# Kernel tuning notes

Measured on AMD Instinct MI355X. Metric: run time of the kernel, lower is better.

## Reference

```python
import jax, jax.numpy as jnp
import numpy as np

N = 50000      # nodes
E = 800000     # edges (before self-loops)
IN_DIM = 256
HID = 128
HEADS = 2
OUT = 64
NEG_SLOPE = 0.2  # PyG GATConv default


def setup_inputs() -> dict:
    key = jax.random.key(0)
    ks = jax.random.split(key, 10)
    x = jax.random.normal(ks[0], (N, IN_DIM), dtype=jnp.float32)
    edge_index = jax.random.randint(ks[1], (2, E), 0, N, dtype=jnp.int64)
    s = 0.05
    return {
        "x": x,
        "edge_index": edge_index,
        "W1": jax.random.normal(ks[2], (IN_DIM, HEADS * HID), dtype=jnp.float32) * s,
        "a_src1": jax.random.normal(ks[3], (HEADS, HID), dtype=jnp.float32) * s,
        "a_dst1": jax.random.normal(ks[4], (HEADS, HID), dtype=jnp.float32) * s,
        "b1": jnp.zeros((HEADS * HID,), dtype=jnp.float32),
        "W2": jax.random.normal(ks[5], (HEADS * HID, OUT), dtype=jnp.float32) * s,
        "a_src2": jax.random.normal(ks[6], (1, OUT), dtype=jnp.float32) * s,
        "a_dst2": jax.random.normal(ks[7], (1, OUT), dtype=jnp.float32) * s,
        "b2": jnp.zeros((OUT,), dtype=jnp.float32),
    }


def _gat_layer(x, src, dst, W, a_src, a_dst, num_nodes):
    """One GATConv (PyG semantics): returns [N, heads, out_per_head]."""
    heads = a_src.shape[0]
    h = (x @ W).reshape(num_nodes, heads, -1)          # [N, H, F]
    alpha_src = jnp.einsum("nhf,hf->nh", h, a_src)     # [N, H]
    alpha_dst = jnp.einsum("nhf,hf->nh", h, a_dst)     # [N, H]
    e = jax.nn.leaky_relu(alpha_src[src] + alpha_dst[dst], NEG_SLOPE)  # [E, H]
    # segment softmax over incoming edges of each destination node
    m = jax.ops.segment_max(e, dst, num_segments=num_nodes)           # [N, H]
    p = jnp.exp(e - m[dst])                                           # [E, H]
    s = jax.ops.segment_sum(p, dst, num_segments=num_nodes)           # [N, H]
    alpha = p / s[dst]                                                # [E, H]
    msg = alpha[:, :, None] * h[src]                                  # [E, H, F]
    return jax.ops.segment_sum(msg, dst, num_segments=num_nodes)      # [N, H, F]


def reference(x, edge_index, W1, a_src1, a_dst1, b1, W2, a_src2, a_dst2, b2):
    num_nodes = x.shape[0]
    # PyG GATConv default add_self_loops=True
    loops = jnp.arange(num_nodes, dtype=edge_index.dtype)
    src = jnp.concatenate([edge_index[0], loops])
    dst = jnp.concatenate([edge_index[1], loops])

    h1 = _gat_layer(x, src, dst, W1, a_src1, a_dst1, num_nodes)   # [N, 2, 128]
    h1 = h1.reshape(num_nodes, -1) + b1                            # concat heads
    h1 = jax.nn.elu(h1)

    h2 = _gat_layer(h1, src, dst, W2, a_src2, a_dst2, num_nodes)  # [N, 1, 64]
    return h2[:, 0, :] + b2
```

## Files before the change

kernel.cpp:

```cpp
#include <hip/hip_runtime.h>
#include <cmath>
#include <cstdint>
#include <cstddef>

#define N_NODES 50000
#define N_EDGES 800000
#define EN_TOT  (N_EDGES + N_NODES)
#define PAD     96
#define F1 256
#define F2 64

typedef __attribute__((ext_vector_type(8))) short short8;
typedef __attribute__((ext_vector_type(4))) float float4v;

__device__ __forceinline__ float bf2f(unsigned short u) {
    return __uint_as_float((unsigned)u << 16);
}
__device__ __forceinline__ unsigned short f2bf(float f) {
    unsigned u = __float_as_uint(f);
    unsigned r = (u + 0x7FFFu + ((u >> 16) & 1u)) >> 16;
    return (unsigned short)r;
}
__device__ __forceinline__ float lrelu(float x) { return x > 0.f ? x : 0.2f * x; }

__global__ void init_kernel(const float* __restrict__ W1, const float* __restrict__ W2,
                            unsigned short* __restrict__ Wt1, unsigned short* __restrict__ Wt2,
                            int* __restrict__ cnt) {
    int idx = blockIdx.x * 256 + threadIdx.x;
    if (idx < N_NODES) cnt[idx] = 0;
    if (idx < 256 * F1) {
        int n = idx / 256, k = idx % 256;
        Wt1[idx] = f2bf(W1[(size_t)k * F1 + n]);
    } else {
        int j = idx - 256 * F1;
        if (j < 256 * F2) {
            int n = j / 256, k = j % 256;
            Wt2[j] = f2bf(W2[(size_t)k * F2 + n]);
        }
    }
}

__global__ void fill_kernel(const int* __restrict__ ei, int* __restrict__ cnt,
                            int* __restrict__ col) {
    int e = blockIdx.x * 256 + threadIdx.x;
    if (e >= EN_TOT) return;
    int src, dst;
    if (e < N_EDGES) { src = ei[e]; dst = ei[N_EDGES + e]; }
    else             { src = dst = e - N_EDGES; }
    int pos = atomicAdd(&cnt[dst], 1);
    if (pos < PAD) col[dst * PAD + pos] = src;
}

__global__ __launch_bounds__(256)
void gemm1_kernel(const float* __restrict__ A, const unsigned short* __restrict__ Bt,
                  unsigned short* __restrict__ Cbf,
                  const float* __restrict__ a_src, const float* __restrict__ a_dst,
                  float* __restrict__ asrc, float* __restrict__ adst, int M) {
    constexpr int BM = 128, BN = 128, BK = 64, K = 256;
    constexpr int FM = 2, FN = 8;
    __shared__ short As[BM * BK];
    __shared__ short Bs[BN * BK];
    const int tid = threadIdx.x;
    const int lane = tid & 63, wid = tid >> 6;
    const int RW = wid * 32;
    const int head = blockIdx.y;
    const int brow = blockIdx.x * BM, bcol = head * BN;
    const int lr = lane & 15, lkg = lane >> 4;

    float4v acc[FM][FN];
    #pragma unroll
    for (int m = 0; m < FM; ++m)
        #pragma unroll
        for (int n = 0; n < FN; ++n) acc[m][n] = (float4v){0.f, 0.f, 0.f, 0.f};

    for (int k0 = 0; k0 < K; k0 += BK) {
        #pragma unroll
        for (int p = 0; p < BM * BK / 1024; ++p) {
            int flat = (p * 256 + tid) * 4;
            int r = flat / BK, kk = flat % BK;
            int gr = brow + r;
            float4 v = make_float4(0.f, 0.f, 0.f, 0.f);
            if (gr < M) v = *(const float4*)&A[(size_t)gr * K + k0 + kk];
            ushort4 o;
            o.x = f2bf(v.x); o.y = f2bf(v.y); o.z = f2bf(v.z); o.w = f2bf(v.w);
            *(ushort4*)((char*)As + r * (BK * 2) + ((kk * 2) ^ ((r & 7) << 4))) = o;
        }
        #pragma unroll
        for (int p = 0; p < BN * BK / 2048; ++p) {
            int flat = (p * 256 + tid) * 8;
            int r = flat / BK, kk = flat % BK;
            short8 v = *(const short8*)&Bt[(size_t)(bcol + r) * K + k0 + kk];
            *(short8*)((char*)Bs + r * (BK * 2) + ((kk * 2) ^ ((r & 7) << 4))) = v;
        }
        __syncthreads();
        #pragma unroll
        for (int ks = 0; ks < 2; ++ks) {
            short8 af[FM], bfr[FN];
            #pragma unroll
            for (int m = 0; m < FM; ++m) {
                int row = RW + m * 16 + lr;
                af[m] = *(const short8*)((const char*)As + row * (BK * 2) +
                        (((ks * 32 + lkg * 8) * 2) ^ ((row & 7) << 4)));
            }
            #pragma unroll
            for (int n = 0; n < FN; ++n) {
                int row = n * 16 + lr;
                bfr[n] = *(const short8*)((const char*)Bs + row * (BK * 2) +
                        (((ks * 32 + lkg * 8) * 2) ^ ((row & 7) << 4)));
            }
            #pragma unroll
            for (int m = 0; m < FM; ++m)
                #pragma unroll
                for (int n = 0; n < FN; ++n)
                    acc[m][n] = __builtin_amdgcn_mfma_f32_16x16x32_bf16(
                        af[m], bfr[n], acc[m][n], 0, 0, 0);
        }
        __syncthreads();
    }
    const float* asv = a_src + head * 128;
    const float* adv = a_dst + head * 128;
    #pragma unroll
    for (int m = 0; m < FM; ++m) {
        #pragma unroll
        for (int j = 0; j < 4; ++j) {
            int row = brow + RW + m * 16 + lkg * 4 + j;
            if (row < M) {
                float ps = 0.f, pd = 0.f;
                #pragma unroll
                for (int n = 0; n < FN; ++n) {
                    float v = acc[m][n][j];
                    int c = n * 16 + lr;
                    Cbf[(size_t)row * F1 + bcol + c] = f2bf(v);
                    ps += v * asv[c];
                    pd += v * adv[c];
                }
                #pragma unroll
                for (int off = 1; off < 16; off <<= 1) {
                    ps += __shfl_xor(ps, off);
                    pd += __shfl_xor(pd, off);
                }
                if (lr == 0) {
                    asrc[row * 2 + head] = ps;
                    adst[row * 2 + head] = pd;
                }
            }
        }
    }
}

__global__ __launch_bounds__(256)
void gemm2_kernel(const unsigned short* __restrict__ A, const unsigned short* __restrict__ Bt,
                  unsigned short* __restrict__ Cbf,
                  const float* __restrict__ a_src, const float* __restrict__ a_dst,
                  float* __restrict__ asrc, float* __restrict__ adst, int M) {
    constexpr int BM = 128, BN = 64, BK = 64, K = 256;
    constexpr int FM = 2, FN = 4;
    __shared__ short As[BM * BK];
    __shared__ short Bs[BN * BK];
    const int tid = threadIdx.x;
    const int lane = tid & 63, wid = tid >> 6;
    const int RW = wid * 32;
    const int brow = blockIdx.x * BM;
    const int lr = lane & 15, lkg = lane >> 4;

    float4v acc[FM][FN];
    #pragma unroll
    for (int m = 0; m < FM; ++m)
        #pragma unroll
        for (int n = 0; n < FN; ++n) acc[m][n] = (float4v){0.f, 0.f, 0.f, 0.f};

    for (int k0 = 0; k0 < K; k0 += BK) {
        #pragma unroll
        for (int p = 0; p < BM * BK / 2048; ++p) {
            int flat = (p * 256 + tid) * 8;
            int r = flat / BK, kk = flat % BK;
            int gr = brow + r;
            short8 v = {0, 0, 0, 0, 0, 0, 0, 0};
            if (gr < M) v = *(const short8*)&A[(size_t)gr * K + k0 + kk];
            *(short8*)((char*)As + r * (BK * 2) + ((kk * 2) ^ ((r & 7) << 4))) = v;
        }
        #pragma unroll
        for (int p = 0; p < BN * BK / 2048; ++p) {
            int flat = (p * 256 + tid) * 8;
            int r = flat / BK, kk = flat % BK;
            short8 v = *(const short8*)&Bt[(size_t)r * K + k0 + kk];
            *(short8*)((char*)Bs + r * (BK * 2) + ((kk * 2) ^ ((r & 7) << 4))) = v;
        }
        __syncthreads();
        #pragma unroll
        for (int ks = 0; ks < 2; ++ks) {
            short8 af[FM], bfr[FN];
            #pragma unroll
            for (int m = 0; m < FM; ++m) {
                int row = RW + m * 16 + lr;
                af[m] = *(const short8*)((const char*)As + row * (BK * 2) +
                        (((ks * 32 + lkg * 8) * 2) ^ ((row & 7) << 4)));
            }
            #pragma unroll
            for (int n = 0; n < FN; ++n) {
                int row = n * 16 + lr;
                bfr[n] = *(const short8*)((const char*)Bs + row * (BK * 2) +
                        (((ks * 32 + lkg * 8) * 2) ^ ((row & 7) << 4)));
            }
            #pragma unroll
            for (int m = 0; m < FM; ++m)
                #pragma unroll
                for (int n = 0; n < FN; ++n)
                    acc[m][n] = __builtin_amdgcn_mfma_f32_16x16x32_bf16(
                        af[m], bfr[n], acc[m][n], 0, 0, 0);
        }
        __syncthreads();
    }
    #pragma unroll
    for (int m = 0; m < FM; ++m) {
        #pragma unroll
        for (int j = 0; j < 4; ++j) {
            int row = brow + RW + m * 16 + lkg * 4 + j;
            if (row < M) {
                float ps = 0.f, pd = 0.f;
                #pragma unroll
                for (int n = 0; n < FN; ++n) {
                    float v = acc[m][n][j];
                    int c = n * 16 + lr;
                    Cbf[(size_t)row * F2 + c] = f2bf(v);
                    ps += v * a_src[c];
                    pd += v * a_dst[c];
                }
                #pragma unroll
                for (int off = 1; off < 16; off <<= 1) {
                    ps += __shfl_xor(ps, off);
                    pd += __shfl_xor(pd, off);
                }
                if (lr == 0) {
                    asrc[row] = ps;
                    adst[row] = pd;
                }
            }
        }
    }
}

__global__ __launch_bounds__(256)
void agg1_kernel(const unsigned short* __restrict__ h_bf,
                 const float* __restrict__ asrc, const float* __restrict__ adst,
                 const int* __restrict__ cnt, const int* __restrict__ col,
                 const float* __restrict__ b1, unsigned short* __restrict__ h1_bf) {
    int n = blockIdx.x * 4 + (threadIdx.x >> 6);
    if (n >= N_NODES) return;
    int lane = threadIdx.x & 63;
    int beg = n * PAD;
    int deg = min(cnt[n], PAD);
    int end = beg + deg;
    float ad0 = adst[2 * n], ad1 = adst[2 * n + 1];

    if (deg <= 64) {
        bool act = lane < deg;
        int src = 0; float e0 = -INFINITY, e1 = -INFINITY;
        if (act) {
            src = col[beg + lane];
            float2 av = *(const float2*)(asrc + 2 * src);
            e0 = lrelu(av.x + ad0); e1 = lrelu(av.y + ad1);
        }
        float m0 = e0, m1 = e1;
        #pragma unroll
        for (int off = 32; off; off >>= 1) {
            m0 = fmaxf(m0, __shfl_xor(m0, off));
            m1 = fmaxf(m1, __shfl_xor(m1, off));
        }
        float p0 = act ? __expf(e0 - m0) : 0.f;
        float p1 = act ? __expf(e1 - m1) : 0.f;
        float s0 = p0, s1 = p1;
        #pragma unroll
        for (int off = 32; off; off >>= 1) {
            s0 += __shfl_xor(s0, off);
            s1 += __shfl_xor(s1, off);
        }
        float w0 = p0 / s0, w1 = p1 / s1;

        int half = lane >> 5, fl = lane & 31;
        bool myhead = fl >= 16;
        float a[8] = {0.f, 0.f, 0.f, 0.f, 0.f, 0.f, 0.f, 0.f};
        for (int i = 0; i < deg; i += 2) {
            int ei = i + half;
            bool ok = ei < deg;
            int eidx = ok ? ei : 0;
            float wa = __shfl(w0, eidx), wb = __shfl(w1, eidx);
            int s = __shfl(src, eidx);
            float w = myhead ? wb : wa;
            if (!ok) w = 0.f;
            short8 v = *(const short8*)(h_bf + (size_t)s * F1 + fl * 8);
            #pragma unroll
            for (int j = 0; j < 8; ++j) a[j] += w * bf2f((unsigned short)v[j]);
        }
        #pragma unroll
        for (int j = 0; j < 8; ++j) a[j] += __shfl_xor(a[j], 32);
        if (half == 0) {
            float bb[8];
            *(float4*)&bb[0] = *(const float4*)(b1 + fl * 8);
            *(float4*)&bb[4] = *(const float4*)(b1 + fl * 8 + 4);
            short8 o;
            #pragma unroll
            for (int j = 0; j < 8; ++j) {
                float v = a[j] + bb[j];
                v = v > 0.f ? v : expm1f(v);
                o[j] = (short)f2bf(v);
            }
            *(short8*)(h1_bf + (size_t)n * F1 + fl * 8) = o;
        }
    } else {
        float a0 = 0.f, a1 = 0.f, a2 = 0.f, a3 = 0.f;
        float m0 = -INFINITY, s0 = 0.f, m1 = -INFINITY, s1 = 0.f;
        for (int k = beg + lane; k < end; k += 64) {
            int src = col[k];
            float2 av = *(const float2*)(asrc + 2 * src);
            float e0 = lrelu(av.x + ad0), e1 = lrelu(av.y + ad1);
            float nm = fmaxf(m0, e0); s0 = s0 * __expf(m0 - nm) + __expf(e0 - nm); m0 = nm;
            nm = fmaxf(m1, e1); s1 = s1 * __expf(m1 - nm) + __expf(e1 - nm); m1 = nm;
        }
        #pragma unroll
        for (int off = 32; off; off >>= 1) {
            float om = __shfl_xor(m0, off), os = __shfl_xor(s0, off);
            float nm = fmaxf(m0, om);
            s0 = (nm == -INFINITY) ? 0.f : (s0 * __expf(m0 - nm) + os * __expf(om - nm));
            m0 = nm;
            om = __shfl_xor(m1, off); os = __shfl_xor(s1, off);
            nm = fmaxf(m1, om);
            s1 = (nm == -INFINITY) ? 0.f : (s1 * __expf(m1 - nm) + os * __expf(om - nm));
            m1 = nm;
        }
        float i0 = 1.f / s0, i1 = 1.f / s1;
        for (int base = beg; base < end; base += 64) {
            int k = base + lane;
            bool act2 = k < end;
            int src = 0; float w0 = 0.f, w1 = 0.f;
            if (act2) {
                src = col[k];
                float2 av = *(const float2*)(asrc + 2 * src);
                w0 = __expf(lrelu(av.x + ad0) - m0) * i0;
                w1 = __expf(lrelu(av.y + ad1) - m1) * i1;
            }
            int cnt2 = min(64, end - base);
            for (int i = 0; i < cnt2; ++i) {
                float wa = __shfl(w0, i), wb = __shfl(w1, i);
                int s = __shfl(src, i);
                float w = (lane >= 32) ? wb : wa;
                ushort4 v = *(const ushort4*)(h_bf + (size_t)s * F1 + lane * 4);
                a0 += w * bf2f(v.x); a1 += w * bf2f(v.y);
                a2 += w * bf2f(v.z); a3 += w * bf2f(v.w);
            }
        }
        const float4 bb = *(const float4*)(b1 + lane * 4);
        float v0 = a0 + bb.x, v1 = a1 + bb.y, v2 = a2 + bb.z, v3 = a3 + bb.w;
        v0 = v0 > 0.f ? v0 : expm1f(v0);
        v1 = v1 > 0.f ? v1 : expm1f(v1);
        v2 = v2 > 0.f ? v2 : expm1f(v2);
        v3 = v3 > 0.f ? v3 : expm1f(v3);
        ushort4 o; o.x = f2bf(v0); o.y = f2bf(v1); o.z = f2bf(v2); o.w = f2bf(v3);
        *(ushort4*)(h1_bf + (size_t)n * F1 + lane * 4) = o;
    }
}

__global__ __launch_bounds__(256)
void agg2_kernel(const unsigned short* __restrict__ g_bf,
                 const float* __restrict__ asrc, const float* __restrict__ adst,
                 const int* __restrict__ cnt, const int* __restrict__ col,
                 const float* __restrict__ b2, float* __restrict__ out) {
    int n = blockIdx.x * 8 + (threadIdx.x >> 5);
    if (n >= N_NODES) return;
    int l = threadIdx.x & 31;
    int lbase = threadIdx.x & 32;
    int beg = n * PAD;
    int deg = min(cnt[n], PAD);
    int end = beg + deg;
    float ad = adst[n];

    if (deg <= 32) {
        bool act = l < deg;
        int src = 0; float e = -INFINITY;
        if (act) {
            src = col[beg + l];
            e = lrelu(asrc[src] + ad);
        }
        float m = e;
        #pragma unroll
        for (int off = 16; off; off >>= 1) m = fmaxf(m, __shfl_xor(m, off));
        float p = act ? __expf(e - m) : 0.f;
        float s = p;
        #pragma unroll
        for (int off = 16; off; off >>= 1) s += __shfl_xor(s, off);
        float w = p / s;

        int sub = l >> 4, fl = l & 15;
        float a0 = 0.f, a1 = 0.f, a2 = 0.f, a3 = 0.f;
        for (int i = 0; i < deg; i += 2) {
            int ei = i + sub;
            bool ok = ei < deg;
            int eidx = ok ? ei : 0;
            float wi = __shfl(w, lbase + eidx);
            int si = __shfl(src, lbase + eidx);
            if (!ok) wi = 0.f;
            ushort4 v = *(const ushort4*)(g_bf + (size_t)si * F2 + fl * 4);
            a0 += wi * bf2f(v.x); a1 += wi * bf2f(v.y);
            a2 += wi * bf2f(v.z); a3 += wi * bf2f(v.w);
        }
        a0 += __shfl_xor(a0, 16); a1 += __shfl_xor(a1, 16);
        a2 += __shfl_xor(a2, 16); a3 += __shfl_xor(a3, 16);
        if (sub == 0) {
            float4 bb = *(const float4*)(b2 + fl * 4);
            float4 o;
            o.x = a0 + bb.x; o.y = a1 + bb.y; o.z = a2 + bb.z; o.w = a3 + bb.w;
            *(float4*)&out[(size_t)n * F2 + fl * 4] = o;
        }
    } else {
        float c0 = 0.f, c1 = 0.f;
        float m = -INFINITY, s = 0.f;
        for (int k = beg + l; k < end; k += 32) {
            int src = col[k];
            float e = lrelu(asrc[src] + ad);
            float nm = fmaxf(m, e);
            s = s * __expf(m - nm) + __expf(e - nm); m = nm;
        }
        #pragma unroll
        for (int off = 16; off; off >>= 1) {
            float om = __shfl_xor(m, off), os = __shfl_xor(s, off);
            float nm = fmaxf(m, om);
            s = (nm == -INFINITY) ? 0.f : (s * __expf(m - nm) + os * __expf(om - nm));
            m = nm;
        }
        float inv = 1.f / s;
        for (int base = beg; base < end; base += 32) {
            int k = base + l;
            bool act2 = k < end;
            int src = 0; float w = 0.f;
            if (act2) {
                src = col[k];
                w = __expf(lrelu(asrc[src] + ad) - m) * inv;
            }
            int cnt2 = min(32, end - base);
            for (int i = 0; i < cnt2; ++i) {
                float wi = __shfl(w, lbase + i);
                int si = __shfl(src, lbase + i);
                ushort2 v = *(const ushort2*)(g_bf + (size_t)si * F2 + l * 2);
                c0 += wi * bf2f(v.x);
                c1 += wi * bf2f(v.y);
            }
        }
        float2 bb = *(const float2*)(b2 + l * 2);
        float2 o; o.x = c0 + bb.x; o.y = c1 + bb.y;
        *(float2*)&out[(size_t)n * F2 + l * 2] = o;
    }
}

extern "C" void kernel_launch(void* const* d_in, const int* in_sizes, int n_in,
                              void* d_out, int out_size, void* d_ws, size_t ws_size,
                              hipStream_t stream) {
    const float* x      = (const float*)d_in[0];
    const int*   ei     = (const int*)d_in[1];
    const float* W1     = (const float*)d_in[2];
    const float* a_src1 = (const float*)d_in[3];
    const float* a_dst1 = (const float*)d_in[4];
    const float* b1     = (const float*)d_in[5];
    const float* W2     = (const float*)d_in[6];
    const float* a_src2 = (const float*)d_in[7];
    const float* a_dst2 = (const float*)d_in[8];
    const float* b2     = (const float*)d_in[9];
    float* out = (float*)d_out;

    char* ws = (char*)d_ws;
    size_t off = 0;
    auto alloc = [&](size_t bytes) -> void* {
        void* p = ws + off;
        off = (off + bytes + 255) & ~(size_t)255;
        return p;
    };
    unsigned short* h_bf   = (unsigned short*)alloc((size_t)N_NODES * F1 * 2);
    unsigned short* h1_bf  = (unsigned short*)alloc((size_t)N_NODES * F1 * 2);
    unsigned short* g_bf   = (unsigned short*)alloc((size_t)N_NODES * F2 * 2);
    unsigned short* Wt1_bf = (unsigned short*)alloc((size_t)F1 * 256 * 2);
    unsigned short* Wt2_bf = (unsigned short*)alloc((size_t)F2 * 256 * 2);
    float* asrc1  = (float*)alloc((size_t)N_NODES * 2 * 4);
    float* adst1  = (float*)alloc((size_t)N_NODES * 2 * 4);
    float* asrc2  = (float*)alloc((size_t)N_NODES * 4);
    float* adst2  = (float*)alloc((size_t)N_NODES * 4);
    int*   cnt    = (int*)alloc((size_t)N_NODES * 4);
    int*   col    = (int*)alloc((size_t)N_NODES * PAD * 4);

    const int eb = (EN_TOT + 255) / 256;
    const int ib = (256 * (F1 + F2) + 255) / 256;
    const int mb = (N_NODES + 127) / 128;
    const int nb4 = (N_NODES + 3) / 4;
    const int nb8 = (N_NODES + 7) / 8;

    init_kernel<<<ib, 256, 0, stream>>>(W1, W2, Wt1_bf, Wt2_bf, cnt);
    fill_kernel<<<eb, 256, 0, stream>>>(ei, cnt, col);

    gemm1_kernel<<<dim3(mb, 2), 256, 0, stream>>>(x, Wt1_bf, h_bf, a_src1, a_dst1,
                                                  asrc1, adst1, N_NODES);
    agg1_kernel<<<nb4, 256, 0, stream>>>(h_bf, asrc1, adst1, cnt, col, b1, h1_bf);

    gemm2_kernel<<<mb, 256, 0, stream>>>(h1_bf, Wt2_bf, g_bf, a_src2, a_dst2,
                                         asrc2, adst2, N_NODES);
    agg2_kernel<<<nb8, 256, 0, stream>>>(g_bf, asrc2, adst2, cnt, col, b2, out);
}
```

Before: 218.7 us.

## Fuse CSR fill into GEMM1 launch as extra blocks to overlap work

```diff
diff --git a/kernel.cpp b/kernel.cpp
--- a/kernel.cpp
+++ b/kernel.cpp
@@ -24,10 +24,8 @@
 __device__ __forceinline__ float lrelu(float x) { return x > 0.f ? x : 0.2f * x; }
 
 __global__ void init_kernel(const float* __restrict__ W1, const float* __restrict__ W2,
-                            unsigned short* __restrict__ Wt1, unsigned short* __restrict__ Wt2,
-                            int* __restrict__ cnt) {
+                            unsigned short* __restrict__ Wt1, unsigned short* __restrict__ Wt2) {
     int idx = blockIdx.x * 256 + threadIdx.x;
-    if (idx < N_NODES) cnt[idx] = 0;
     if (idx < 256 * F1) {
         int n = idx / 256, k = idx % 256;
         Wt1[idx] = f2bf(W1[(size_t)k * F1 + n]);
@@ -40,22 +38,25 @@
     }
 }
 
-__global__ void fill_kernel(const int* __restrict__ ei, int* __restrict__ cnt,
-                            int* __restrict__ col) {
-    int e = blockIdx.x * 256 + threadIdx.x;
-    if (e >= EN_TOT) return;
-    int src, dst;
-    if (e < N_EDGES) { src = ei[e]; dst = ei[N_EDGES + e]; }
-    else             { src = dst = e - N_EDGES; }
-    int pos = atomicAdd(&cnt[dst], 1);
-    if (pos < PAD) col[dst * PAD + pos] = src;
-}
-
+#define GEMM_BLOCKS 782
 __global__ __launch_bounds__(256)
-void gemm1_kernel(const float* __restrict__ A, const unsigned short* __restrict__ Bt,
+void mega1_kernel(const float* __restrict__ A, const unsigned short* __restrict__ Bt,
                   unsigned short* __restrict__ Cbf,
                   const float* __restrict__ a_src, const float* __restrict__ a_dst,
-                  float* __restrict__ asrc, float* __restrict__ adst, int M) {
+                  float* __restrict__ asrc, float* __restrict__ adst, int M,
+                  const int* __restrict__ ei, int* __restrict__ cnt,
+                  int* __restrict__ col) {
+    if (blockIdx.x >= GEMM_BLOCKS) {
+        int e = (blockIdx.x - GEMM_BLOCKS) * 256 + threadIdx.x;
+        if (e < EN_TOT) {
+            int src, dst;
+            if (e < N_EDGES) { src = ei[e]; dst = ei[N_EDGES + e]; }
+            else             { src = dst = e - N_EDGES; }
+            int pos = atomicAdd(&cnt[dst], 1);
+            if (pos < PAD) col[dst * PAD + pos] = src;
+        }
+        return;
+    }
     constexpr int BM = 128, BN = 128, BK = 64, K = 256;
     constexpr int FM = 2, FN = 8;
     __shared__ short As[BM * BK];
@@ -63,8 +64,8 @@
     const int tid = threadIdx.x;
     const int lane = tid & 63, wid = tid >> 6;
     const int RW = wid * 32;
-    const int head = blockIdx.y;
-    const int brow = blockIdx.x * BM, bcol = head * BN;
+    const int head = blockIdx.x & 1;
+    const int brow = (blockIdx.x >> 1) * BM, bcol = head * BN;
     const int lr = lane & 15, lkg = lane >> 4;
 
     float4v acc[FM][FN];
@@ -485,17 +486,18 @@
     int*   cnt    = (int*)alloc((size_t)N_NODES * 4);
     int*   col    = (int*)alloc((size_t)N_NODES * PAD * 4);
 
-    const int eb = (EN_TOT + 255) / 256;
+    const int fb = (EN_TOT + 255) / 256;
     const int ib = (256 * (F1 + F2) + 255) / 256;
     const int mb = (N_NODES + 127) / 128;
     const int nb4 = (N_NODES + 3) / 4;
     const int nb8 = (N_NODES + 7) / 8;
 
-    init_kernel<<<ib, 256, 0, stream>>>(W1, W2, Wt1_bf, Wt2_bf, cnt);
-    fill_kernel<<<eb, 256, 0, stream>>>(ei, cnt, col);
-
-    gemm1_kernel<<<dim3(mb, 2), 256, 0, stream>>>(x, Wt1_bf, h_bf, a_src1, a_dst1,
-                                                  asrc1, adst1, N_NODES);
+    hipMemsetAsync(cnt, 0, (size_t)N_NODES * 4, stream);
+    init_kernel<<<ib, 256, 0, stream>>>(W1, W2, Wt1_bf, Wt2_bf);
+
+    mega1_kernel<<<GEMM_BLOCKS + fb, 256, 0, stream>>>(
+        x, Wt1_bf, h_bf, a_src1, a_dst1, asrc1, adst1, N_NODES, ei, cnt, col);
+
     agg1_kernel<<<nb4, 256, 0, stream>>>(h_bf, asrc1, adst1, cnt, col, b1, h1_bf);
 
     gemm2_kernel<<<mb, 256, 0, stream>>>(h1_bf, Wt2_bf, g_bf, a_src2, a_dst2,
```

Result: faster. 182.0 us (-16.7%).
